# Performance work log

Measured on AMD Instinct MI355X. Metric: run time of the kernel, lower is better.

## Reference

```python
import jax, jax.numpy as jnp
import numpy as np

B, IN, H, K = 4096, 1024, 1024, 32  # batch, input_size, hidden_size, inner_hidden


def setup_inputs() -> dict:
    key = jax.random.key(0)
    ks = jax.random.split(key, 11)
    stdv = 1.0 / np.sqrt(H)
    u = lambda k, shp: jax.random.uniform(k, shp, jnp.float32, -stdv, stdv)
    return {
        "x": jax.random.normal(ks[0], (B, IN), jnp.float32),
        "h_prev": jax.random.normal(ks[1], (B, H), jnp.float32),
        "c_prev": jax.random.normal(ks[2], (B, H), jnp.float32),
        "Wg": u(ks[3], (3 * H, IN + H)),
        "bg": u(ks[4], (3 * H,)),
        "Wc": u(ks[5], (2 * H, IN + H)),
        "bc": u(ks[6], (2 * H,)),
        "W1": u(ks[7], (K, 2)),
        "b1": u(ks[8], (K,)),
        "W2": u(ks[9], (1, K)),
        "b2": u(ks[10], (1,)),
    }


def reference(x, h_prev, c_prev, Wg, bg, Wc, bc, W1, b1, W2, b2):
    combined = jnp.concatenate([x, h_prev], axis=1)          # [B, IN+H]
    gates = combined @ Wg.T + bg                              # [B, 3H]
    i, f, o = jnp.split(jax.nn.sigmoid(gates), 3, axis=1)     # each [B, H]
    cell_raw = combined @ Wc.T + bc                           # [B, 2H]
    pairs = cell_raw.reshape(B, H, 2)                         # [B, H, 2]
    hid = jax.nn.relu(jnp.einsum('bhp,kp->bhk', pairs, W1) + b1)  # [B, H, K]
    g = jnp.einsum('bhk,ok->bho', hid, W2)[..., 0] + b2[0]    # [B, H]
    c_next = f * c_prev + i * g
    h_next = o * jnp.tanh(c_next)
    return (h_next, c_next)
```

## Files before the change

kernel.cpp:

```cpp
#include <hip/hip_runtime.h>
#include <hip/hip_bf16.h>

#define BB   4096
#define INW  1024
#define HH   1024
#define KIN  2048
#define NG   5120
#define KH   32
#define FPG  10
#define NTG  32

typedef __bf16 bf16;
typedef __bf16 bf16x4 __attribute__((ext_vector_type(4)));
typedef __bf16 bf16x8 __attribute__((ext_vector_type(8)));
typedef float  floatx4 __attribute__((ext_vector_type(4)));

#define GLD16(gp, lp)                                                          \
  __builtin_amdgcn_global_load_lds(                                            \
      (__attribute__((address_space(1))) const void*)(gp),                     \
      (__attribute__((address_space(3))) void*)(lp), 16, 0, 0)

#define NCB  4096
#define NWB  1280

__global__ __launch_bounds__(256) void prep(
    const float* __restrict__ x, const float* __restrict__ h,
    const float* __restrict__ Wg, const float* __restrict__ Wc,
    bf16* __restrict__ comb, bf16* __restrict__ Wb) {
  int tid = threadIdx.x;
  if (blockIdx.x < NCB) {
    int e = (blockIdx.x * 256 + tid) * 8;
    int b = e >> 11;
    int c = e & (KIN - 1);
    const float* src = (c < INW) ? (x + (size_t)b * INW + c)
                                 : (h + (size_t)b * HH + (c - INW));
    float4 v0 = *(const float4*)src;
    float4 v1 = *(const float4*)(src + 4);
    bf16x8 ov;
    ov[0] = (bf16)v0.x; ov[1] = (bf16)v0.y; ov[2] = (bf16)v0.z; ov[3] = (bf16)v0.w;
    ov[4] = (bf16)v1.x; ov[5] = (bf16)v1.y; ov[6] = (bf16)v1.z; ov[7] = (bf16)v1.w;
    *(bf16x8*)(comb + e) = ov;
  } else {
    int w   = blockIdx.x - NCB;
    int nt  = w / 40;
    int rem = w - nt * 40;
    int f   = rem >> 2;
    int rp  = rem & 3;
    int q   = f / 5;
    int g   = f - q * 5;
    int kk  = tid >> 2;
    int kq  = tid & 3;
    size_t wbase = ((size_t)(nt * FPG + f) * 64 + kk) * 64 + kq * 16;
#pragma unroll
    for (int r4 = 0; r4 < 4; ++r4) {
      int s    = rp * 4 + r4;
      int hcol = nt * 32 + q * 16 + s;
      const float* src = (g < 3)
          ? (Wg + (size_t)(g * HH + hcol) * KIN + tid * 8)
          : (Wc + (size_t)(2 * hcol + (g - 3)) * KIN + tid * 8);
      float4 v0 = *(const float4*)src;
      float4 v1 = *(const float4*)(src + 4);
      bf16x8 ov;
      ov[0] = (bf16)v0.x; ov[1] = (bf16)v0.y; ov[2] = (bf16)v0.z; ov[3] = (bf16)v0.w;
      ov[4] = (bf16)v1.x; ov[5] = (bf16)v1.y; ov[6] = (bf16)v1.z; ov[7] = (bf16)v1.w;
      *(bf16x8*)(Wb + (wbase + s) * 8) = ov;
    }
  }
}

#define ASZ  8192

__global__ __launch_bounds__(256, 2) void gemm_fused(
    const bf16* __restrict__ A, const bf16* __restrict__ Bm,
    const float* __restrict__ c_prev, const float* __restrict__ bg,
    const float* __restrict__ bc, const float* __restrict__ W1,
    const float* __restrict__ b1, const float* __restrict__ W2,
    const float* __restrict__ b2, float* __restrict__ h_next,
    float* __restrict__ c_next) {
  __shared__ bf16 As2[4 * ASZ];

  const int tid  = threadIdx.x;
  const int wave = tid >> 6;
  const int lane = tid & 63;

  const int bid = blockIdx.y * gridDim.x + blockIdx.x;
  const int swz = (bid & 7) * 128 + (bid >> 3);
  const int m0  = (swz & 31) * 128;
  const int nt  = swz >> 5;

  const int wm = (wave >> 1) * 64;
  const int q  = wave & 1;
  const int lr = lane & 15;
  const int qd = lane >> 4;

  const bf16* Bq = Bm + (size_t)(nt * FPG + q * 5) * 32768 + (size_t)lane * 8;

  floatx4 acc[4][5] = {};
  bf16x8 bregA[2][5], bregB[2][5];

  const int arow0 = tid >> 3;
  const int acol  = tid & 7;

#define LOADB(buf, kt)                                                         \
  {                                                                            \
    _Pragma("unroll")                                                          \
    for (int ks = 0; ks < 2; ++ks)                                             \
      _Pragma("unroll")                                                        \
      for (int ni = 0; ni < 5; ++ni)                                           \
        buf[ks][ni] = *(const bf16x8*)(Bq + (size_t)ni * 32768 +               \
                                       (size_t)((kt) * 2 + ks) * 512);         \
  }

#define STAGEA(bb, kt)                                                         \
  {                                                                            \
    _Pragma("unroll")                                                          \
    for (int j = 0; j < 4; ++j) {                                              \
      int row = arow0 + j * 32;                                                \
      int c   = acol ^ (row & 7);                                              \
      GLD16(A + (size_t)(m0 + row) * KIN + (kt) * 64 + c * 8,                  \
            As2 + (size_t)(bb) * ASZ + (size_t)(j * 256 + wave * 64) * 8);     \
    }                                                                          \
  }

#define COMPUTE(bb, buf)                                                       \
  {                                                                            \
    const bf16* As = As2 + (size_t)(bb) * ASZ;                                 \
    _Pragma("unroll")                                                          \
    for (int ks = 0; ks < 2; ++ks) {                                           \
      bf16x8 af[4];                                                            \
      _Pragma("unroll")                                                        \
      for (int mi = 0; mi < 4; ++mi) {                                         \
        int row  = wm + mi * 16 + lr;                                          \
        int slot = (ks * 4 + qd) ^ (lr & 7);                                   \
        af[mi] = *(const bf16x8*)&As[(row << 6) + (slot << 3)];                \
      }                                                                        \
      _Pragma("unroll")                                                        \
      for (int mi = 0; mi < 4; ++mi)                                           \
        _Pragma("unroll")                                                      \
        for (int ni = 0; ni < 5; ++ni)                                         \
          acc[mi][ni] = __builtin_amdgcn_mfma_f32_16x16x32_bf16(               \
              af[mi], buf[ks][ni], acc[mi][ni], 0, 0, 0);                      \
    }                                                                          \
  }

#define ITER(u, bnext, bcur, t)                                                \
  {                                                                            \
    int tb = ((t) + 1 < 32) ? (t) + 1 : 31;          \
    LOADB(bnext, tb);                                                          \
    asm volatile("s_waitcnt vmcnt(14)" ::: "memory");                          \
    __builtin_amdgcn_s_barrier();                                              \
    __builtin_amdgcn_sched_barrier(0);                                         \
    int ta = ((t) + 2 < 32) ? (t) + 2 : 31;          \
    STAGEA(((u) + 2) & 3, ta);                                                 \
    COMPUTE((u), bcur);                                                        \
  }

  STAGEA(0, 0);
  STAGEA(1, 1);
  LOADB(bregA, 0);
  asm volatile("s_waitcnt vmcnt(0)" ::: "memory");
  __builtin_amdgcn_s_barrier();
  __builtin_amdgcn_sched_barrier(0);

#pragma unroll 1
  for (int trip = 0; trip < 8; ++trip) {
    const int t0 = trip * 4;
    ITER(0, bregB, bregA, t0 + 0);
    ITER(1, bregA, bregB, t0 + 1);
    ITER(2, bregB, bregA, t0 + 2);
    ITER(3, bregA, bregB, t0 + 3);
  }

  asm volatile("s_waitcnt vmcnt(0)" ::: "memory");

  const int h   = nt * 32 + q * 16 + lr;
  const float bgi = bg[h];
  const float bgf = bg[HH + h];
  const float bgo = bg[2 * HH + h];
  const float bc0 = bc[2 * h];
  const float bc1 = bc[2 * h + 1];
  const float gb  = b2[0];

  float p0[16], p1[16], ga[16];
#pragma unroll
  for (int mi = 0; mi < 4; ++mi)
#pragma unroll
    for (int r = 0; r < 4; ++r) {
      p0[mi * 4 + r] = acc[mi][3][r] + bc0;
      p1[mi * 4 + r] = acc[mi][4][r] + bc1;
      ga[mi * 4 + r] = gb;
    }
#pragma unroll
  for (int k = 0; k < KH; ++k) {
    float w0 = W1[2 * k], w1 = W1[2 * k + 1], bk = b1[k], wk = W2[k];
#pragma unroll
    for (int e = 0; e < 16; ++e) {
      float hv = fmaf(p0[e], w0, fmaf(p1[e], w1, bk));
      hv = fmaxf(hv, 0.0f);
      ga[e] = fmaf(hv, wk, ga[e]);
    }
  }

#pragma unroll
  for (int mi = 0; mi < 4; ++mi)
#pragma unroll
    for (int r = 0; r < 4; ++r) {
      int b    = m0 + wm + mi * 16 + qd * 4 + r;
      size_t o = (size_t)b * HH + h;
      float si = 1.0f / (1.0f + __expf(-(acc[mi][0][r] + bgi)));
      float sf = 1.0f / (1.0f + __expf(-(acc[mi][1][r] + bgf)));
      float so = 1.0f / (1.0f + __expf(-(acc[mi][2][r] + bgo)));
      float cn = fmaf(sf, c_prev[o], si * ga[mi * 4 + r]);
      float e2 = __expf(2.0f * cn);
      float th = 1.0f - 2.0f / (e2 + 1.0f);
      h_next[o] = so * th;
      c_next[o] = cn;
    }
}

extern "C" void kernel_launch(void* const* d_in, const int* in_sizes, int n_in,
                              void* d_out, int out_size, void* d_ws, size_t ws_size,
                              hipStream_t stream) {
  const float* x      = (const float*)d_in[0];
  const float* h_prev = (const float*)d_in[1];
  const float* c_prev = (const float*)d_in[2];
  const float* Wg     = (const float*)d_in[3];
  const float* bg     = (const float*)d_in[4];
  const float* Wc     = (const float*)d_in[5];
  const float* bc     = (const float*)d_in[6];
  const float* W1     = (const float*)d_in[7];
  const float* b1     = (const float*)d_in[8];
  const float* W2     = (const float*)d_in[9];
  const float* b2     = (const float*)d_in[10];
  float* out = (float*)d_out;

  char* ws = (char*)d_ws;
  bf16* comb = (bf16*)ws;
  bf16* Wb   = (bf16*)(ws + (size_t)BB * KIN * 2);

  prep<<<NCB + NWB, 256, 0, stream>>>(x, h_prev, Wg, Wc, comb, Wb);

  dim3 grid(BB / 128, NTG);
  gemm_fused<<<grid, 256, 0, stream>>>(comb, Wb, c_prev, bg, bc, W1, b1, W2,
                                       b2, out, out + (size_t)BB * HH);
}
```

Before: 257.2 us.

## Use 512-thread blocks with smaller per-wave tiles and simpler B loading

Doubles the gemm block size to 8 waves, each computing 32 rows instead of 64, which halves the accumulators and A fragments per wave. The B-fragment register double-buffer is removed: B is now loaded for the current k-step and waited on just before compute. A staging prefetch depth drops from two stages to one. The aim is to cut register pressure and add latency-hiding waves. In exchange, B global loads are duplicated across more waves, B latency is no longer overlapped with compute, and LDS use (64KB per block) may cap how many blocks fit per CU.

```diff
diff --git a/kernel.cpp b/kernel.cpp
--- a/kernel.cpp
+++ b/kernel.cpp
@@ -70,7 +70,7 @@
 
 #define ASZ  8192
 
-__global__ __launch_bounds__(256, 2) void gemm_fused(
+__global__ __launch_bounds__(512, 4) void gemm_fused(
     const bf16* __restrict__ A, const bf16* __restrict__ Bm,
     const float* __restrict__ c_prev, const float* __restrict__ bg,
     const float* __restrict__ bc, const float* __restrict__ W1,
@@ -88,87 +88,82 @@
   const int m0  = (swz & 31) * 128;
   const int nt  = swz >> 5;
 
-  const int wm = (wave >> 1) * 64;
+  const int wm = (wave >> 1) * 32;
   const int q  = wave & 1;
   const int lr = lane & 15;
   const int qd = lane >> 4;
 
   const bf16* Bq = Bm + (size_t)(nt * FPG + q * 5) * 32768 + (size_t)lane * 8;
 
-  floatx4 acc[4][5] = {};
-  bf16x8 bregA[2][5], bregB[2][5];
-
-  const int arow0 = tid >> 3;
-  const int acol  = tid & 7;
-
-#define LOADB(buf, kt)                                                         \
+  floatx4 acc[2][5] = {};
+  bf16x8 bfr[2][5];
+
+  const int as0 = tid;
+
+#define LOADB(kt)                                                              \
   {                                                                            \
     _Pragma("unroll")                                                          \
     for (int ks = 0; ks < 2; ++ks)                                             \
       _Pragma("unroll")                                                        \
       for (int ni = 0; ni < 5; ++ni)                                           \
-        buf[ks][ni] = *(const bf16x8*)(Bq + (size_t)ni * 32768 +               \
+        bfr[ks][ni] = *(const bf16x8*)(Bq + (size_t)ni * 32768 +               \
                                        (size_t)((kt) * 2 + ks) * 512);         \
   }
 
 #define STAGEA(bb, kt)                                                         \
   {                                                                            \
     _Pragma("unroll")                                                          \
-    for (int j = 0; j < 4; ++j) {                                              \
-      int row = arow0 + j * 32;                                                \
-      int c   = acol ^ (row & 7);                                              \
+    for (int j = 0; j < 2; ++j) {                                              \
+      int s   = j * 512 + as0;                                                 \
+      int row = s >> 3;                                                        \
+      int c   = (s & 7) ^ (row & 7);                                           \
       GLD16(A + (size_t)(m0 + row) * KIN + (kt) * 64 + c * 8,                  \
-            As2 + (size_t)(bb) * ASZ + (size_t)(j * 256 + wave * 64) * 8);     \
+            As2 + (size_t)(bb) * ASZ + (size_t)(j * 512 + wave * 64) * 8);     \
     }                                                                          \
   }
 
-#define COMPUTE(bb, buf)                                                       \
+#define COMPUTE(bb)                                                            \
   {                                                                            \
     const bf16* As = As2 + (size_t)(bb) * ASZ;                                 \
     _Pragma("unroll")                                                          \
     for (int ks = 0; ks < 2; ++ks) {                                           \
-      bf16x8 af[4];                                                            \
+      bf16x8 af[2];                                                            \
       _Pragma("unroll")                                                        \
-      for (int mi = 0; mi < 4; ++mi) {                                         \
+      for (int mi = 0; mi < 2; ++mi) {                                         \
         int row  = wm + mi * 16 + lr;                                          \
         int slot = (ks * 4 + qd) ^ (lr & 7);                                   \
         af[mi] = *(const bf16x8*)&As[(row << 6) + (slot << 3)];                \
       }                                                                        \
       _Pragma("unroll")                                                        \
-      for (int mi = 0; mi < 4; ++mi)                                           \
+      for (int mi = 0; mi < 2; ++mi)                                           \
         _Pragma("unroll")                                                      \
         for (int ni = 0; ni < 5; ++ni)                                         \
           acc[mi][ni] = __builtin_amdgcn_mfma_f32_16x16x32_bf16(               \
-              af[mi], buf[ks][ni], acc[mi][ni], 0, 0, 0);                      \
+              af[mi], bfr[ks][ni], acc[mi][ni], 0, 0, 0);                      \
     }                                                                          \
   }
 
-#define ITER(u, bnext, bcur, t)                                                \
-  {                                                                            \
-    int tb = ((t) + 1 < 32) ? (t) + 1 : 31;          \
-    LOADB(bnext, tb);                                                          \
-    asm volatile("s_waitcnt vmcnt(14)" ::: "memory");                          \
+#define ITER(u, t)                                                             \
+  {                                                                            \
+    LOADB(t);                                         \
+    __builtin_amdgcn_sched_barrier(0);                                         \
+    int ta = ((t) + 1 < 32) ? (t) + 1 : 31;         \
+    STAGEA(((u) + 1) & 3, ta);                          \
+    asm volatile("s_waitcnt vmcnt(2)" ::: "memory");       \
     __builtin_amdgcn_s_barrier();                                              \
     __builtin_amdgcn_sched_barrier(0);                                         \
-    int ta = ((t) + 2 < 32) ? (t) + 2 : 31;          \
-    STAGEA(((u) + 2) & 3, ta);                                                 \
-    COMPUTE((u), bcur);                                                        \
+    COMPUTE(u);                                                                \
   }
 
   STAGEA(0, 0);
-  STAGEA(1, 1);
-  LOADB(bregA, 0);
-  asm volatile("s_waitcnt vmcnt(0)" ::: "memory");
-  __builtin_amdgcn_s_barrier();
-  __builtin_amdgcn_sched_barrier(0);
 
 #pragma unroll 1
   for (int trip = 0; trip < 8; ++trip) {
     const int t0 = trip * 4;
-    ITER(0, bregB, bregA, t0 + 0);
-    ITER(1, bregA, bregB, t0 + 1);
-    ITER(2, bregB, bregA, t0 + 2);
-    ITER(3, bregA, bregB, t0 + 3);
+    ITER(0, t0 + 0);
+    ITER(1, t0 + 1);
+    ITER(2, t0 + 2);
+    ITER(3, t0 + 3);
   }
 
   asm volatile("s_waitcnt vmcnt(0)" ::: "memory");
@@ -181,9 +176,9 @@
   const float bc1 = bc[2 * h + 1];
   const float gb  = b2[0];
 
-  float p0[16], p1[16], ga[16];
-#pragma unroll
-  for (int mi = 0; mi < 4; ++mi)
+  float p0[8], p1[8], ga[8];
+#pragma unroll
+  for (int mi = 0; mi < 2; ++mi)
 #pragma unroll
     for (int r = 0; r < 4; ++r) {
       p0[mi * 4 + r] = acc[mi][3][r] + bc0;
@@ -194,7 +189,7 @@
   for (int k = 0; k < KH; ++k) {
     float w0 = W1[2 * k], w1 = W1[2 * k + 1], bk = b1[k], wk = W2[k];
 #pragma unroll
-    for (int e = 0; e < 16; ++e) {
+    for (int e = 0; e < 8; ++e) {
       float hv = fmaf(p0[e], w0, fmaf(p1[e], w1, bk));
       hv = fmaxf(hv, 0.0f);
       ga[e] = fmaf(hv, wk, ga[e]);
@@ -202,7 +197,7 @@
   }
 
 #pragma unroll
-  for (int mi = 0; mi < 4; ++mi)
+  for (int mi = 0; mi < 2; ++mi)
 #pragma unroll
     for (int r = 0; r < 4; ++r) {
       int b    = m0 + wm + mi * 16 + qd * 4 + r;
@@ -241,6 +236,6 @@
   prep<<<NCB + NWB, 256, 0, stream>>>(x, h_prev, Wg, Wc, comb, Wb);
 
   dim3 grid(BB / 128, NTG);
-  gemm_fused<<<grid, 256, 0, stream>>>(comb, Wb, c_prev, bg, bc, W1, b1, W2,
+  gemm_fused<<<grid, 512, 0, stream>>>(comb, Wb, c_prev, bg, bc, W1, b1, W2,
                                        b2, out, out + (size_t)BB * HH);
 }
```

Result: slower. 277.4 us (+7.8%).
